# Kernel optimization log

Measured on AMD Instinct MI355X. Metric: run time of the kernel, lower is better.

Reference implementation:

```python
import jax, jax.numpy as jnp
import numpy as np

NUM_HEADS = 16
NUM_KV_GROUPS = 4
EPS = 1e-6


def _rms_norm(x, w):
    # normalize over last dim (head_dim)
    return x * jax.lax.rsqrt(jnp.mean(x * x, axis=-1, keepdims=True) + EPS) * w


def _rope_cos_sin(T, head_dim):
    half = head_dim // 2
    inv_freq = 1.0 / (10000.0 ** (jnp.arange(half, dtype=jnp.float32) / half))
    freqs = jnp.arange(T, dtype=jnp.float32)[:, None] * inv_freq[None, :]  # [T, half]
    cos = jnp.repeat(jnp.cos(freqs), 2, axis=-1)  # [T, head_dim]
    sin = jnp.repeat(jnp.sin(freqs), 2, axis=-1)
    return cos, sin


def _apply_rope(x, cos, sin):
    # x: [B, H, T, head_dim]; cos/sin broadcast over B,H
    x1 = x[..., ::2]
    x2 = x[..., 1::2]
    x_rot = jnp.stack([-x2, x1], axis=-1).reshape(x.shape)  # interleave (-x2, x1)
    return x * cos + x_rot * sin


def setup_inputs() -> dict:
    key = jax.random.key(0)
    ks = jax.random.split(key, 5)
    scale = lambda k, sh: jax.random.normal(k, sh, dtype=jnp.float32) * 0.02
    return {
        "x": jax.random.normal(ks[0], (4, 2048, 1024), dtype=jnp.float32),
        "Wq": scale(ks[1], (1024, 1024)),
        "Wk": scale(ks[2], (256, 1024)),
        "Wv": scale(ks[3], (256, 1024)),
        "Wo": scale(ks[4], (1024, 1024)),
        "qn_w": jnp.ones((64,), jnp.float32),
        "kn_w": jnp.ones((64,), jnp.float32),
    }


def reference(x, Wq, Wk, Wv, Wo, qn_w, kn_w):
    B, T, D = x.shape
    H, G = NUM_HEADS, NUM_KV_GROUPS
    hd = D // H

    # projections (torch Linear: y = x @ W.T), reshape to [B, heads, T, hd]
    q = (x @ Wq.T).reshape(B, T, H, hd).transpose(0, 2, 1, 3)
    k = (x @ Wk.T).reshape(B, T, G, hd).transpose(0, 2, 1, 3)
    v = (x @ Wv.T).reshape(B, T, G, hd).transpose(0, 2, 1, 3)

    # optional qk RMSNorm (qk_norm=True)
    q = _rms_norm(q, qn_w)
    k = _rms_norm(k, kn_w)

    # RoPE (position_offset = 0)
    cos, sin = _rope_cos_sin(T, hd)
    q = _apply_rope(q, cos, sin)
    k = _apply_rope(k, cos, sin)

    # GQA: expand kv heads to match query heads
    rep = H // G
    k = jnp.repeat(k, rep, axis=1)
    v = jnp.repeat(v, rep, axis=1)

    # causal SDPA
    scores = jnp.einsum('bhqd,bhkd->bhqk', q, k) / jnp.sqrt(jnp.float32(hd))
    causal = jnp.tril(jnp.ones((T, T), dtype=bool))
    scores = jnp.where(causal, scores, jnp.float32(-1e30))
    attn = jax.nn.softmax(scores, axis=-1)
    out = jnp.einsum('bhqk,bhkd->bhqd', attn, v)

    out = out.transpose(0, 2, 1, 3).reshape(B, T, D)
    return out @ Wo.T
```

## Files before the change

### kernel.cpp

```cpp
#include <hip/hip_runtime.h>

typedef unsigned short u16;
typedef __attribute__((ext_vector_type(8))) short bf16x8;
typedef __attribute__((ext_vector_type(4))) short bf16x4;
typedef __attribute__((ext_vector_type(4))) float f32x4;

#define GP(p) ((const __attribute__((address_space(1))) void*)(unsigned long long)(p))
#define LP(p) ((__attribute__((address_space(3))) void*)(unsigned int)(unsigned long long)(p))

#define QSCALE 0.180336879486998f
#define M_BIAS (-12.0f)

__device__ __forceinline__ u16 f2bf(float f) {
  union { float f; unsigned u; } v; v.f = f;
  unsigned r = v.u + 0x7fffu + ((v.u >> 16) & 1u);
  return (u16)(r >> 16);
}
__device__ __forceinline__ short f2bf_cvt(float f) {
  __bf16 b = (__bf16)f;
  return *reinterpret_cast<short*>(&b);
}

#if __has_builtin(__builtin_amdgcn_mfma_f32_16x16x16bf16_1k)
#define MFMA16(A, B, C) __builtin_amdgcn_mfma_f32_16x16x16bf16_1k((A), (B), (C), 0, 0, 0)
#elif __has_builtin(__builtin_amdgcn_mfma_f32_16x16x16_bf16)
#define MFMA16(A, B, C) __builtin_amdgcn_mfma_f32_16x16x16_bf16((A), (B), (C), 0, 0, 0)
#else
static __device__ __forceinline__ f32x4 mfma16_asm(bf16x4 a, bf16x4 b, f32x4 c) {
  asm volatile("v_mfma_f32_16x16x16_bf16 %0, %1, %2, %0" : "+v"(c) : "v"(a), "v"(b));
  return c;
}
#define MFMA16(A, B, C) mfma16_asm((A), (B), (C))
#endif

__global__ void cast_kernel(const float* __restrict__ in, u16* __restrict__ out, int n4) {
  int i = blockIdx.x * blockDim.x + threadIdx.x;
  int stride = gridDim.x * blockDim.x;
  for (; i < n4; i += stride) {
    float4 v = reinterpret_cast<const float4*>(in)[i];
    ushort4 o = make_ushort4(f2bf(v.x), f2bf(v.y), f2bf(v.z), f2bf(v.w));
    reinterpret_cast<ushort4*>(out)[i] = o;
  }
}

__global__ void cast_w_kernel(const float* __restrict__ Wq, const float* __restrict__ Wk,
                              const float* __restrict__ Wv, const float* __restrict__ Wo,
                              u16* __restrict__ Wcat, u16* __restrict__ Wob) {
  int i = blockIdx.x * 256 + threadIdx.x;
  const float* src; u16* dst; int off;
  if (i < 262144)      { src = Wq; dst = Wcat;           off = i; }
  else if (i < 327680) { src = Wk; dst = Wcat + 1048576; off = i - 262144; }
  else if (i < 393216) { src = Wv; dst = Wcat + 1310720; off = i - 327680; }
  else                 { src = Wo; dst = Wob;            off = i - 393216; }
  float4 v = reinterpret_cast<const float4*>(src)[off];
  reinterpret_cast<ushort4*>(dst)[off] =
      make_ushort4(f2bf(v.x), f2bf(v.y), f2bf(v.z), f2bf(v.w));
}

__global__ void rope_table_kernel(float* __restrict__ ctab, float* __restrict__ stab) {
  int i = blockIdx.x * 256 + threadIdx.x;
  int t = i >> 5, f = i & 31;
  float inv = exp2f((float)f * (-13.287712379549449f / 32.0f));
  float ang = (float)t * inv;
  float sv, cv;
  sincosf(ang, &sv, &cv);
  ctab[i] = cv;
  stab[i] = sv;
}

__launch_bounds__(256)
__global__ void gemm_qkv_kernel(const u16* __restrict__ A, const u16* __restrict__ W,
                                u16* __restrict__ qh, u16* __restrict__ kh,
                                u16* __restrict__ vt,
                                const float* __restrict__ qn_w, const float* __restrict__ kn_w,
                                const float* __restrict__ ctab, const float* __restrict__ stab) {
  __shared__ __align__(16) u16 As[128 * 64];
  __shared__ __align__(16) u16 Bs[128 * 64];
  const int tid = threadIdx.x;
  const int w = tid >> 6, l = tid & 63;
  const int lr = l & 15, lk = l >> 4;
  const int wr = w >> 1, wc = w & 1;
  const int m0 = blockIdx.x * 128, n0 = blockIdx.y * 128;
  f32x4 acc[4][4] = {};
  for (int k0 = 0; k0 < 1024; k0 += 64) {
#pragma unroll
    for (int i = 0; i < 4; ++i) {
      int c = i * 256 + tid;
      const u16* ga = A + (size_t)(m0 + (c >> 3)) * 1024 + k0 + (c & 7) * 8;
      __builtin_amdgcn_global_load_lds(GP(ga), LP((char*)As + (i * 256 + (tid & ~63)) * 16), 16, 0, 0);
      const u16* gb = W + (size_t)(n0 + (c >> 3)) * 1024 + k0 + (c & 7) * 8;
      __builtin_amdgcn_global_load_lds(GP(gb), LP((char*)Bs + (i * 256 + (tid & ~63)) * 16), 16, 0, 0);
    }
    asm volatile("s_waitcnt vmcnt(0)" ::: "memory");
    __syncthreads();
#pragma unroll
    for (int kk = 0; kk < 2; ++kk) {
      bf16x8 af[4], bfr[4];
#pragma unroll
      for (int fi = 0; fi < 4; ++fi)
        af[fi] = *reinterpret_cast<const bf16x8*>(&As[(wr * 64 + fi * 16 + lr) * 64 + kk * 32 + lk * 8]);
#pragma unroll
      for (int fj = 0; fj < 4; ++fj)
        bfr[fj] = *reinterpret_cast<const bf16x8*>(&Bs[(wc * 64 + fj * 16 + lr) * 64 + kk * 32 + lk * 8]);
#pragma unroll
      for (int fi = 0; fi < 4; ++fi)
#pragma unroll
        for (int fj = 0; fj < 4; ++fj)
          acc[fi][fj] = __builtin_amdgcn_mfma_f32_16x16x32_bf16(af[fi], bfr[fj], acc[fi][fj], 0, 0, 0);
    }
    __syncthreads();
  }
  const int ncol0 = n0 + wc * 64;
  if (ncol0 < 1280) {
    const bool isq = ncol0 < 1024;
    const float* wn = isq ? qn_w : kn_w;
    const float sc = isq ? QSCALE : 1.0f;
    float wv[4];
#pragma unroll
    for (int fj = 0; fj < 4; ++fj) wv[fj] = wn[fj * 16 + lr];
#pragma unroll
    for (int fi = 0; fi < 4; ++fi)
#pragma unroll
      for (int r = 0; r < 4; ++r) {
        float ss = 0.f;
#pragma unroll
        for (int fj = 0; fj < 4; ++fj) ss += acc[fi][fj][r] * acc[fi][fj][r];
        ss += __shfl_xor(ss, 1); ss += __shfl_xor(ss, 2);
        ss += __shfl_xor(ss, 4); ss += __shfl_xor(ss, 8);
        float rinv = rsqrtf(ss * (1.0f / 64.0f) + 1e-6f);
        int m = m0 + wr * 64 + fi * 16 + lk * 4 + r;
        int t = m & 2047, b = m >> 11;
#pragma unroll
        for (int fj = 0; fj < 4; ++fj) {
          float xn = acc[fi][fj][r] * rinv * wv[fj];
          float pr = __shfl_xor(xn, 1);
          float rot = (lr & 1) ? pr : -pr;
          int ci = t * 32 + fj * 8 + (lr >> 1);
          u16 outv = f2bf((xn * ctab[ci] + rot * stab[ci]) * sc);
          int n = ncol0 + fj * 16 + lr;
          if (isq) {
            int h = n >> 6, d = n & 63;
            qh[((size_t)((b * 16 + h) * 2048 + t)) * 64 + d] = outv;
          } else {
            int n2 = n - 1024, g = n2 >> 6, d = n2 & 63;
            kh[((size_t)((b * 4 + g) * 2048 + t)) * 64 + d] = outv;
          }
        }
      }
  } else {
#pragma unroll
    for (int fi = 0; fi < 4; ++fi)
#pragma unroll
      for (int fj = 0; fj < 4; ++fj) {
        int m = m0 + wr * 64 + fi * 16 + lk * 4;
        int b = m >> 11, t = m & 2047;
        int n2 = ncol0 + fj * 16 + lr - 1280;
        int g = n2 >> 6, d = n2 & 63;
        bf16x4 o;
#pragma unroll
        for (int r = 0; r < 4; ++r) o[r] = f2bf_cvt(acc[fi][fj][r]);
        *reinterpret_cast<bf16x4*>(&vt[((size_t)((b * 4 + g) * 64 + d)) * 2048 + t]) = o;
      }
  }
}

__launch_bounds__(256)
__global__ void attn_kernel(const u16* __restrict__ qh, const u16* __restrict__ kh,
                            const u16* __restrict__ vt, u16* __restrict__ ao) {
  __shared__ __align__(16) u16 Ks[2][64 * 64];
  __shared__ __align__(16) u16 Vts[2][64 * 64];
  const int tid = threadIdx.x, w = tid >> 6, l = tid & 63;
  const int lr = l & 15, lk = l >> 4;
  const int id = blockIdx.y * 16 + blockIdx.x;
  const int vid = (id & 7) * 128 + (id >> 3);
  const int p = vid & 15, bh = vid >> 4;
  const int b = bh >> 4, h = bh & 15, g = h >> 2;
  const u16* Qh = qh + ((size_t)((b * 16 + h) * 2048)) * 64;
  const u16* Kb = kh + ((size_t)((b * 4 + g) * 2048)) * 64;
  const u16* Vtb = vt + ((size_t)((b * 4 + g) * 64)) * 2048;
  const int swz = (lr & 7) * 8;

  const int c1 = 256 + tid;
  const int r0 = tid >> 3, s0 = ((tid & 7) ^ (r0 & 7)) * 8;
  const int r1 = c1 >> 3, s1 = ((c1 & 7) ^ (r1 & 7)) * 8;
  char* kd = (char*)&Ks[0][0] + (tid & ~63) * 16;
  char* vd = (char*)&Vts[0][0] + (tid & ~63) * 16;
  const u16* kp0; const u16* kp1; const u16* vp0; const u16* vp1;

  auto stage = [&](int buf) {
    __builtin_amdgcn_global_load_lds(GP(kp0), LP(kd + buf * 8192), 16, 0, 0);
    __builtin_amdgcn_global_load_lds(GP(kp1), LP(kd + buf * 8192 + 4096), 16, 0, 0);
    __builtin_amdgcn_global_load_lds(GP(vp0), LP(vd + buf * 8192), 16, 0, 0);
    __builtin_amdgcn_global_load_lds(GP(vp1), LP(vd + buf * 8192 + 4096), 16, 0, 0);
    kp0 += 64 * 64; kp1 += 64 * 64; vp0 += 64; vp1 += 64;
  };

  int cur = 0;
  auto run_qtile = [&](int qt) {
    const int q0 = qt * 64;
    const u16* Qb = Qh + (size_t)(q0 + w * 16) * 64;
    const bf16x8 qf0 = *reinterpret_cast<const bf16x8*>(&Qb[lr * 64 + lk * 8]);
    const bf16x8 qf1 = *reinterpret_cast<const bf16x8*>(&Qb[lr * 64 + 32 + lk * 8]);
    f32x4 oacc[4] = {};
    float lrow = 0.f;
    kp0 = Kb + r0 * 64 + s0;
    kp1 = Kb + r1 * 64 + s1;
    vp0 = Vtb + (size_t)r0 * 2048 + s0;
    vp1 = Vtb + (size_t)r1 * 2048 + s1;
    stage(cur);
    asm volatile("s_waitcnt vmcnt(0)" ::: "memory");
    __builtin_amdgcn_s_barrier();
    for (int it = 0; it <= qt; ++it) {
      if (it < qt) stage(cur ^ 1);
      f32x4 sacc[4];
#pragma unroll
      for (int fi = 0; fi < 4; ++fi)
#pragma unroll
        for (int r = 0; r < 4; ++r) sacc[fi][r] = M_BIAS;
      __builtin_amdgcn_s_setprio(1);
#pragma unroll
      for (int kk = 0; kk < 2; ++kk) {
        bf16x8 qf = kk ? qf1 : qf0;
#pragma unroll
        for (int fi = 0; fi < 4; ++fi) {
          bf16x8 kf = *reinterpret_cast<const bf16x8*>(
              &Ks[cur][(fi * 16 + lr) * 64 + ((kk * 32 + lk * 8) ^ swz)]);
          sacc[fi] = __builtin_amdgcn_mfma_f32_16x16x32_bf16(kf, qf, sacc[fi], 0, 0, 0);
        }
      }
      __builtin_amdgcn_s_setprio(0);
      if (it == qt) {
        int qloc = w * 16 + lr;
#pragma unroll
        for (int fi = 0; fi < 4; ++fi)
#pragma unroll
          for (int r = 0; r < 4; ++r)
            if (fi * 16 + lk * 4 + r > qloc) sacc[fi][r] = -1e30f;
      }
      bf16x4 pb[4];
#pragma unroll
      for (int fi = 0; fi < 4; ++fi)
#pragma unroll
        for (int r = 0; r < 4; ++r) {
          float pv = exp2f(sacc[fi][r]);
          lrow += pv;
          pb[fi][r] = f2bf_cvt(pv);
        }
      __builtin_amdgcn_s_setprio(1);
#pragma unroll
      for (int fi = 0; fi < 4; ++fi)
#pragma unroll
        for (int db = 0; db < 4; ++db) {
          bf16x4 vf = *reinterpret_cast<const bf16x4*>(
              &Vts[cur][(db * 16 + lr) * 64 + ((fi * 16 + lk * 4) ^ swz)]);
          oacc[db] = MFMA16(vf, pb[fi], oacc[db]);
        }
      __builtin_amdgcn_s_setprio(0);
      asm volatile("s_waitcnt vmcnt(0)" ::: "memory");
      __builtin_amdgcn_s_barrier();
      cur ^= 1;
    }
    float lsum = lrow;
    lsum += __shfl_xor(lsum, 16);
    lsum += __shfl_xor(lsum, 32);
    float inv = 1.0f / lsum;
#pragma unroll
    for (int db = 0; db < 4; ++db) {
      bf16x4 o;
#pragma unroll
      for (int r = 0; r < 4; ++r) o[r] = f2bf_cvt(oacc[db][r] * inv);
      *reinterpret_cast<bf16x4*>(
          &ao[((size_t)(b * 2048 + q0 + w * 16 + lr)) * 1024 + h * 64 + db * 16 + lk * 4]) = o;
    }
  };
  run_qtile(31 - p);
  run_qtile(p);
}

__launch_bounds__(256)
__global__ void gemm_out_kernel(const u16* __restrict__ A, const u16* __restrict__ W,
                                float* __restrict__ out) {
  __shared__ __align__(16) u16 As[128 * 64];
  __shared__ __align__(16) u16 Bs[128 * 64];
  const int tid = threadIdx.x;
  const int w = tid >> 6, l = tid & 63;
  const int lr = l & 15, lk = l >> 4;
  const int wr = w >> 1, wc = w & 1;
  const int m0 = blockIdx.x * 128, n0 = blockIdx.y * 128;
  f32x4 acc[4][4] = {};
  for (int k0 = 0; k0 < 1024; k0 += 64) {
#pragma unroll
    for (int i = 0; i < 4; ++i) {
      int c = i * 256 + tid;
      const u16* ga = A + (size_t)(m0 + (c >> 3)) * 1024 + k0 + (c & 7) * 8;
      __builtin_amdgcn_global_load_lds(GP(ga), LP((char*)As + (i * 256 + (tid & ~63)) * 16), 16, 0, 0);
      const u16* gb = W + (size_t)(n0 + (c >> 3)) * 1024 + k0 + (c & 7) * 8;
      __builtin_amdgcn_global_load_lds(GP(gb), LP((char*)Bs + (i * 256 + (tid & ~63)) * 16), 16, 0, 0);
    }
    asm volatile("s_waitcnt vmcnt(0)" ::: "memory");
    __syncthreads();
#pragma unroll
    for (int kk = 0; kk < 2; ++kk) {
      bf16x8 af[4], bfr[4];
#pragma unroll
      for (int fi = 0; fi < 4; ++fi)
        af[fi] = *reinterpret_cast<const bf16x8*>(&As[(wr * 64 + fi * 16 + lr) * 64 + kk * 32 + lk * 8]);
#pragma unroll
      for (int fj = 0; fj < 4; ++fj)
        bfr[fj] = *reinterpret_cast<const bf16x8*>(&Bs[(wc * 64 + fj * 16 + lr) * 64 + kk * 32 + lk * 8]);
#pragma unroll
      for (int fi = 0; fi < 4; ++fi)
#pragma unroll
        for (int fj = 0; fj < 4; ++fj)
          acc[fi][fj] = __builtin_amdgcn_mfma_f32_16x16x32_bf16(af[fi], bfr[fj], acc[fi][fj], 0, 0, 0);
    }
    __syncthreads();
  }
#pragma unroll
  for (int fi = 0; fi < 4; ++fi)
#pragma unroll
    for (int fj = 0; fj < 4; ++fj)
#pragma unroll
      for (int r = 0; r < 4; ++r) {
        int m = m0 + wr * 64 + fi * 16 + lk * 4 + r;
        int n = n0 + wc * 64 + fj * 16 + lr;
        out[(size_t)m * 1024 + n] = acc[fi][fj][r];
      }
}

extern "C" void kernel_launch(void* const* d_in, const int* in_sizes, int n_in,
                              void* d_out, int out_size, void* d_ws, size_t ws_size,
                              hipStream_t stream) {
  const float* x  = (const float*)d_in[0];
  const float* Wq = (const float*)d_in[1];
  const float* Wk = (const float*)d_in[2];
  const float* Wv = (const float*)d_in[3];
  const float* Wo = (const float*)d_in[4];
  const float* qn = (const float*)d_in[5];
  const float* kn = (const float*)d_in[6];
  float* out = (float*)d_out;
  char* ws = (char*)d_ws;
  u16* xb   = (u16*)(ws);
  u16* Wcat = (u16*)(ws + 16777216);
  u16* Wob  = (u16*)(ws + 19922944);
  u16* qh   = (u16*)(ws + 22020096);
  u16* kh   = (u16*)(ws + 38797312);
  u16* vtb  = (u16*)(ws + 42991616);
  u16* ao   = (u16*)(ws + 47185920);
  float* ctab = (float*)ao;
  float* stab = ctab + 65536;

  cast_kernel<<<2048, 256, 0, stream>>>(x, xb, 8388608 / 4);
  cast_w_kernel<<<2560, 256, 0, stream>>>(Wq, Wk, Wv, Wo, Wcat, Wob);
  rope_table_kernel<<<256, 256, 0, stream>>>(ctab, stab);
  dim3 g1(64, 12);
  gemm_qkv_kernel<<<g1, 256, 0, stream>>>(xb, Wcat, qh, kh, vtb, qn, kn, ctab, stab);
  dim3 ga(16, 64);
  attn_kernel<<<ga, 256, 0, stream>>>(qh, kh, vtb, ao);
  dim3 g2(64, 8);
  gemm_out_kernel<<<g2, 256, 0, stream>>>(ao, Wob, out);
}
```

Before: 180.7 us.

## Share K/V tiles across two GQA heads per 512-thread attention block

The attention kernel now launches 512 blocks of 512 threads. Each block handles two query heads that share a KV group, with four waves per head, and loads each K/V tile into LDS once for both heads. This halves the global-to-LDS staging per head and the staging instructions per thread. In exchange each block is larger, which may reduce scheduling flexibility, and the block-to-XCD mapping is changed.

```diff
diff --git a/kernel.cpp b/kernel.cpp
--- a/kernel.cpp
+++ b/kernel.cpp
@@ -164,49 +164,46 @@
   }
 }
 
-__launch_bounds__(256)
+__launch_bounds__(512)
 __global__ void attn_kernel(const u16* __restrict__ qh, const u16* __restrict__ kh,
                             const u16* __restrict__ vt, u16* __restrict__ ao) {
   __shared__ __align__(16) u16 Ks[2][64 * 64];
   __shared__ __align__(16) u16 Vts[2][64 * 64];
   const int tid = threadIdx.x, w = tid >> 6, l = tid & 63;
   const int lr = l & 15, lk = l >> 4;
-  const int id = blockIdx.y * 16 + blockIdx.x;
-  const int vid = (id & 7) * 128 + (id >> 3);
-  const int p = vid & 15, bh = vid >> 4;
-  const int b = bh >> 4, h = bh & 15, g = h >> 2;
+  const int wq = w & 3, wh = w >> 2;
+  const int D = blockIdx.x;
+  const int j = D >> 3;
+  const int p = j & 15, hp = (j >> 4) & 1;
+  const int z = (D & 7) + 8 * (j >> 5);
+  const int b = z >> 2, g = z & 3;
+  const int h = g * 4 + hp * 2 + wh;
   const u16* Qh = qh + ((size_t)((b * 16 + h) * 2048)) * 64;
-  const u16* Kb = kh + ((size_t)((b * 4 + g) * 2048)) * 64;
-  const u16* Vtb = vt + ((size_t)((b * 4 + g) * 64)) * 2048;
+  const u16* Kb = kh + ((size_t)z * 2048) * 64;
+  const u16* Vtb = vt + ((size_t)z * 64) * 2048;
   const int swz = (lr & 7) * 8;
 
-  const int c1 = 256 + tid;
   const int r0 = tid >> 3, s0 = ((tid & 7) ^ (r0 & 7)) * 8;
-  const int r1 = c1 >> 3, s1 = ((c1 & 7) ^ (r1 & 7)) * 8;
   char* kd = (char*)&Ks[0][0] + (tid & ~63) * 16;
   char* vd = (char*)&Vts[0][0] + (tid & ~63) * 16;
-  const u16* kp0; const u16* kp1; const u16* vp0; const u16* vp1;
+  const u16* kp; const u16* vp;
 
   auto stage = [&](int buf) {
-    __builtin_amdgcn_global_load_lds(GP(kp0), LP(kd + buf * 8192), 16, 0, 0);
-    __builtin_amdgcn_global_load_lds(GP(kp1), LP(kd + buf * 8192 + 4096), 16, 0, 0);
-    __builtin_amdgcn_global_load_lds(GP(vp0), LP(vd + buf * 8192), 16, 0, 0);
-    __builtin_amdgcn_global_load_lds(GP(vp1), LP(vd + buf * 8192 + 4096), 16, 0, 0);
-    kp0 += 64 * 64; kp1 += 64 * 64; vp0 += 64; vp1 += 64;
+    __builtin_amdgcn_global_load_lds(GP(kp), LP(kd + buf * 8192), 16, 0, 0);
+    __builtin_amdgcn_global_load_lds(GP(vp), LP(vd + buf * 8192), 16, 0, 0);
+    kp += 64 * 64; vp += 64;
   };
 
   int cur = 0;
   auto run_qtile = [&](int qt) {
     const int q0 = qt * 64;
-    const u16* Qb = Qh + (size_t)(q0 + w * 16) * 64;
+    const u16* Qb = Qh + (size_t)(q0 + wq * 16) * 64;
     const bf16x8 qf0 = *reinterpret_cast<const bf16x8*>(&Qb[lr * 64 + lk * 8]);
     const bf16x8 qf1 = *reinterpret_cast<const bf16x8*>(&Qb[lr * 64 + 32 + lk * 8]);
     f32x4 oacc[4] = {};
     float lrow = 0.f;
-    kp0 = Kb + r0 * 64 + s0;
-    kp1 = Kb + r1 * 64 + s1;
-    vp0 = Vtb + (size_t)r0 * 2048 + s0;
-    vp1 = Vtb + (size_t)r1 * 2048 + s1;
+    kp = Kb + r0 * 64 + s0;
+    vp = Vtb + (size_t)r0 * 2048 + s0;
     stage(cur);
     asm volatile("s_waitcnt vmcnt(0)" ::: "memory");
     __builtin_amdgcn_s_barrier();
@@ -230,7 +227,7 @@
       }
       __builtin_amdgcn_s_setprio(0);
       if (it == qt) {
-        int qloc = w * 16 + lr;
+        int qloc = wq * 16 + lr;
 #pragma unroll
         for (int fi = 0; fi < 4; ++fi)
 #pragma unroll
@@ -270,7 +267,7 @@
 #pragma unroll
       for (int r = 0; r < 4; ++r) o[r] = f2bf_cvt(oacc[db][r] * inv);
       *reinterpret_cast<bf16x4*>(
-          &ao[((size_t)(b * 2048 + q0 + w * 16 + lr)) * 1024 + h * 64 + db * 16 + lk * 4]) = o;
+          &ao[((size_t)(b * 2048 + q0 + wq * 16 + lr)) * 1024 + h * 64 + db * 16 + lk * 4]) = o;
     }
   };
   run_qtile(31 - p);
@@ -355,8 +352,7 @@
   rope_table_kernel<<<256, 256, 0, stream>>>(ctab, stab);
   dim3 g1(64, 12);
   gemm_qkv_kernel<<<g1, 256, 0, stream>>>(xb, Wcat, qh, kh, vtb, qn, kn, ctab, stab);
-  dim3 ga(16, 64);
-  attn_kernel<<<ga, 256, 0, stream>>>(qh, kh, vtb, ao);
+  attn_kernel<<<512, 512, 0, stream>>>(qh, kh, vtb, ao);
   dim3 g2(64, 8);
   gemm_out_kernel<<<g2, 256, 0, stream>>>(ao, Wob, out);
 }
```

New measurement: 171.5 us. -5.1%, faster.

## Process two query heads per attention block to share K/V tiles

Applied to the files above, without the earlier changes.

Each attention block now handles two query heads of the same GQA group, so every K/V tile staged into LDS serves twice as many MFMAs. The grid drops from 1024 to 512 blocks. The row-sum of probabilities is computed with an MFMA against a ones vector instead of scalar adds plus cross-lane shuffles. This doubles per-thread accumulators and query fragments, which raises register pressure despite the launch-bounds occupancy hint, and halves the block count available to fill the GPU.

```diff
diff --git a/kernel.cpp b/kernel.cpp
--- a/kernel.cpp
+++ b/kernel.cpp
@@ -164,20 +164,23 @@
   }
 }
 
-__launch_bounds__(256)
+__launch_bounds__(256, 4)
 __global__ void attn_kernel(const u16* __restrict__ qh, const u16* __restrict__ kh,
                             const u16* __restrict__ vt, u16* __restrict__ ao) {
   __shared__ __align__(16) u16 Ks[2][64 * 64];
   __shared__ __align__(16) u16 Vts[2][64 * 64];
   const int tid = threadIdx.x, w = tid >> 6, l = tid & 63;
   const int lr = l & 15, lk = l >> 4;
-  const int id = blockIdx.y * 16 + blockIdx.x;
-  const int vid = (id & 7) * 128 + (id >> 3);
-  const int p = vid & 15, bh = vid >> 4;
-  const int b = bh >> 4, h = bh & 15, g = h >> 2;
-  const u16* Qh = qh + ((size_t)((b * 16 + h) * 2048)) * 64;
-  const u16* Kb = kh + ((size_t)((b * 4 + g) * 2048)) * 64;
-  const u16* Vtb = vt + ((size_t)((b * 4 + g) * 64)) * 2048;
+  const int D = blockIdx.x;
+  const int j = D >> 3;
+  const int p = j & 15, hp = (j >> 4) & 1;
+  const int z = (D & 7) + 8 * (j >> 5);
+  const int b = z >> 2, g = z & 3;
+  const int h0 = g * 4 + hp * 2, h1 = h0 + 1;
+  const u16* Qh0 = qh + ((size_t)((b * 16 + h0) * 2048)) * 64;
+  const u16* Qh1 = qh + ((size_t)((b * 16 + h1) * 2048)) * 64;
+  const u16* Kb = kh + ((size_t)z * 2048) * 64;
+  const u16* Vtb = vt + ((size_t)z * 64) * 2048;
   const int swz = (lr & 7) * 8;
 
   const int c1 = 256 + tid;
@@ -195,14 +198,21 @@
     kp0 += 64 * 64; kp1 += 64 * 64; vp0 += 64; vp1 += 64;
   };
 
+  bf16x4 ones;
+#pragma unroll
+  for (int r = 0; r < 4; ++r) ones[r] = (short)0x3F80;
+
   int cur = 0;
   auto run_qtile = [&](int qt) {
     const int q0 = qt * 64;
-    const u16* Qb = Qh + (size_t)(q0 + w * 16) * 64;
-    const bf16x8 qf0 = *reinterpret_cast<const bf16x8*>(&Qb[lr * 64 + lk * 8]);
-    const bf16x8 qf1 = *reinterpret_cast<const bf16x8*>(&Qb[lr * 64 + 32 + lk * 8]);
-    f32x4 oacc[4] = {};
-    float lrow = 0.f;
+    const u16* Qb0 = Qh0 + (size_t)(q0 + w * 16) * 64;
+    const u16* Qb1 = Qh1 + (size_t)(q0 + w * 16) * 64;
+    const bf16x8 qA0 = *reinterpret_cast<const bf16x8*>(&Qb0[lr * 64 + lk * 8]);
+    const bf16x8 qA1 = *reinterpret_cast<const bf16x8*>(&Qb0[lr * 64 + 32 + lk * 8]);
+    const bf16x8 qB0 = *reinterpret_cast<const bf16x8*>(&Qb1[lr * 64 + lk * 8]);
+    const bf16x8 qB1 = *reinterpret_cast<const bf16x8*>(&Qb1[lr * 64 + 32 + lk * 8]);
+    f32x4 oacc0[4] = {}, oacc1[4] = {};
+    f32x4 lacc0 = {}, lacc1 = {};
     kp0 = Kb + r0 * 64 + s0;
     kp1 = Kb + r1 * 64 + s1;
     vp0 = Vtb + (size_t)r0 * 2048 + s0;
@@ -212,20 +222,20 @@
     __builtin_amdgcn_s_barrier();
     for (int it = 0; it <= qt; ++it) {
       if (it < qt) stage(cur ^ 1);
-      f32x4 sacc[4];
-#pragma unroll
-      for (int fi = 0; fi < 4; ++fi)
-#pragma unroll
-        for (int r = 0; r < 4; ++r) sacc[fi][r] = M_BIAS;
+      f32x4 s0a[4], s1a[4];
+#pragma unroll
+      for (int fi = 0; fi < 4; ++fi)
+#pragma unroll
+        for (int r = 0; r < 4; ++r) { s0a[fi][r] = M_BIAS; s1a[fi][r] = M_BIAS; }
       __builtin_amdgcn_s_setprio(1);
 #pragma unroll
       for (int kk = 0; kk < 2; ++kk) {
-        bf16x8 qf = kk ? qf1 : qf0;
 #pragma unroll
         for (int fi = 0; fi < 4; ++fi) {
           bf16x8 kf = *reinterpret_cast<const bf16x8*>(
               &Ks[cur][(fi * 16 + lr) * 64 + ((kk * 32 + lk * 8) ^ swz)]);
-          sacc[fi] = __builtin_amdgcn_mfma_f32_16x16x32_bf16(kf, qf, sacc[fi], 0, 0, 0);
+          s0a[fi] = __builtin_amdgcn_mfma_f32_16x16x32_bf16(kf, kk ? qA1 : qA0, s0a[fi], 0, 0, 0);
+          s1a[fi] = __builtin_amdgcn_mfma_f32_16x16x32_bf16(kf, kk ? qB1 : qB0, s1a[fi], 0, 0, 0);
         }
       }
       __builtin_amdgcn_s_setprio(0);
@@ -235,42 +245,49 @@
         for (int fi = 0; fi < 4; ++fi)
 #pragma unroll
           for (int r = 0; r < 4; ++r)
-            if (fi * 16 + lk * 4 + r > qloc) sacc[fi][r] = -1e30f;
-      }
-      bf16x4 pb[4];
+            if (fi * 16 + lk * 4 + r > qloc) { s0a[fi][r] = -1e30f; s1a[fi][r] = -1e30f; }
+      }
+      bf16x4 pb0[4], pb1[4];
 #pragma unroll
       for (int fi = 0; fi < 4; ++fi)
 #pragma unroll
         for (int r = 0; r < 4; ++r) {
-          float pv = exp2f(sacc[fi][r]);
-          lrow += pv;
-          pb[fi][r] = f2bf_cvt(pv);
+          pb0[fi][r] = f2bf_cvt(exp2f(s0a[fi][r]));
+          pb1[fi][r] = f2bf_cvt(exp2f(s1a[fi][r]));
         }
       __builtin_amdgcn_s_setprio(1);
+#pragma unroll
+      for (int fi = 0; fi < 4; ++fi) {
+        lacc0 = MFMA16(ones, pb0[fi], lacc0);
+        lacc1 = MFMA16(ones, pb1[fi], lacc1);
+      }
 #pragma unroll
       for (int fi = 0; fi < 4; ++fi)
 #pragma unroll
         for (int db = 0; db < 4; ++db) {
           bf16x4 vf = *reinterpret_cast<const bf16x4*>(
               &Vts[cur][(db * 16 + lr) * 64 + ((fi * 16 + lk * 4) ^ swz)]);
-          oacc[db] = MFMA16(vf, pb[fi], oacc[db]);
+          oacc0[db] = MFMA16(vf, pb0[fi], oacc0[db]);
+          oacc1[db] = MFMA16(vf, pb1[fi], oacc1[db]);
         }
       __builtin_amdgcn_s_setprio(0);
       asm volatile("s_waitcnt vmcnt(0)" ::: "memory");
       __builtin_amdgcn_s_barrier();
       cur ^= 1;
     }
-    float lsum = lrow;
-    lsum += __shfl_xor(lsum, 16);
-    lsum += __shfl_xor(lsum, 32);
-    float inv = 1.0f / lsum;
+    float inv0 = 1.0f / lacc0[0];
+    float inv1 = 1.0f / lacc1[0];
 #pragma unroll
     for (int db = 0; db < 4; ++db) {
-      bf16x4 o;
-#pragma unroll
-      for (int r = 0; r < 4; ++r) o[r] = f2bf_cvt(oacc[db][r] * inv);
-      *reinterpret_cast<bf16x4*>(
-          &ao[((size_t)(b * 2048 + q0 + w * 16 + lr)) * 1024 + h * 64 + db * 16 + lk * 4]) = o;
+      bf16x4 o0, o1;
+#pragma unroll
+      for (int r = 0; r < 4; ++r) {
+        o0[r] = f2bf_cvt(oacc0[db][r] * inv0);
+        o1[r] = f2bf_cvt(oacc1[db][r] * inv1);
+      }
+      size_t rowb = ((size_t)(b * 2048 + q0 + w * 16 + lr)) * 1024;
+      *reinterpret_cast<bf16x4*>(&ao[rowb + h0 * 64 + db * 16 + lk * 4]) = o0;
+      *reinterpret_cast<bf16x4*>(&ao[rowb + h1 * 64 + db * 16 + lk * 4]) = o1;
     }
   };
   run_qtile(31 - p);
@@ -355,8 +372,7 @@
   rope_table_kernel<<<256, 256, 0, stream>>>(ctab, stab);
   dim3 g1(64, 12);
   gemm_qkv_kernel<<<g1, 256, 0, stream>>>(xb, Wcat, qh, kh, vtb, qn, kn, ctab, stab);
-  dim3 ga(16, 64);
-  attn_kernel<<<ga, 256, 0, stream>>>(qh, kh, vtb, ao);
+  attn_kernel<<<512, 256, 0, stream>>>(qh, kh, vtb, ao);
   dim3 g2(64, 8);
   gemm_out_kernel<<<g2, 256, 0, stream>>>(ao, Wob, out);
 }
```

Result: no change. 178.4 us (-1.3%).
